# Performance work log

Hardware: AMD Instinct MI355X
Metric: run time of the kernel (lower is better)

The kernel has to match this reference:

```python
import jax, jax.numpy as jnp
import numpy as np

CHUNK = 32  # chunk_size in _delta_rule_chunkwise


def _dwconv_causal(x, filt):
    """Depthwise causal conv. x: [B, L, C], filt: [C, K] -> [B, L, C].
    Matches torch F.conv1d(pad_left=K-1, groups=C) (cross-correlation)."""
    K = filt.shape[-1]
    xc = jnp.transpose(x, (0, 2, 1))  # [B, C, L]
    y = jax.lax.conv_general_dilated(
        xc, filt[:, None, :], (1,), [(K - 1, 0)],
        dimension_numbers=("NCH", "OIH", "NCH"),
        feature_group_count=filt.shape[0])
    return jnp.transpose(y, (0, 2, 1))


def _delta_rule_chunkwise(q, k, v, beta):
    """q,k: [B,H,L,Dk], v: [B,H,L,Dv], beta: [B,H,L]. L % CHUNK == 0."""
    b, h, L, dk = q.shape
    dv = v.shape[-1]
    c = CHUNK
    n = L // c
    q = q * jax.lax.rsqrt(jnp.sum(q * q, -1, keepdims=True))  # l2norm
    k = k * jax.lax.rsqrt(jnp.sum(k * k, -1, keepdims=True))
    v = v * beta[..., None]
    kb = k * beta[..., None]
    qc = q.reshape(b, h, n, c, dk)
    kc = k.reshape(b, h, n, c, dk)
    vc = v.reshape(b, h, n, c, dv)
    kbc = kb.reshape(b, h, n, c, dk)
    # UT transform: T = -(k_beta k^T) strictly-lower, forward substitution, + I
    lower = jnp.tril(jnp.ones((c, c), bool), -1)
    T = -jnp.einsum("bhncd,bhned->bhnce", kbc, kc) * lower
    for i in range(1, c):  # fixed small chunk, sequential dependency
        T = T.at[..., i, :].add(jnp.einsum("bhnj,bhnjk->bhnk", T[..., i, :], T))
    T = T + jnp.eye(c, dtype=T.dtype)
    u = T @ vc   # [b,h,n,c,dv]
    w = T @ kbc  # [b,h,n,c,dk]
    causal = jnp.tril(jnp.ones((c, c), bool))  # incl. diagonal

    def step(S, inp):
        q_i, k_i, u_i, w_i = inp
        attn = jnp.einsum("bhcd,bhed->bhce", q_i, k_i) * causal
        u_t = u_i - w_i @ S
        o_i = q_i @ S + attn @ u_t
        S = S + jnp.einsum("bhcd,bhce->bhde", k_i, u_t)
        return S, o_i

    S0 = jnp.zeros((b, h, dk, dv), q.dtype)
    xs = tuple(jnp.moveaxis(t, 2, 0) for t in (qc, kc, u, w))
    S, o = jax.lax.scan(step, S0, xs)
    o = jnp.moveaxis(o, 0, 2).reshape(b, h, L, dv)
    return o, S


def _rmsnorm(x, weight, eps=1e-5):
    return x * jax.lax.rsqrt(jnp.mean(x * x, -1, keepdims=True) + eps) * weight


def setup_inputs() -> dict:
    B, L, H, NH = 2, 4096, 1024, 4
    DV = H // NH  # 256
    key = jax.random.key(0)
    ks = jax.random.split(key, 14)

    def nrm(k, shape, s=0.02):
        return jax.random.normal(k, shape, jnp.float32) * s

    bf2 = jnp.zeros((NH * 4,), jnp.float32).at[3::4].set(2.0)  # gate_bias_init
    return {
        "hidden_states": jax.random.normal(ks[0], (B, L, H), jnp.float32),
        "Wq": nrm(ks[1], (H, H)), "Wk": nrm(ks[2], (H, H)), "Wv": nrm(ks[3], (H, H)),
        "Wb": nrm(ks[4], (H, NH)),
        "conv_q_w": nrm(ks[5], (H, 4), 0.2),
        "conv_k_w": nrm(ks[6], (H, 4), 0.2),
        "conv_v_w": nrm(ks[7], (H, 4), 0.2),
        "fir_short_w": nrm(ks[8], (NH, DV, 7)),
        "fir_long_w": nrm(ks[9], (NH, DV, 64)),
        "Wf1": nrm(ks[10], (H, 2 * H)), "bf1": jnp.zeros((2 * H,), jnp.float32),
        "Wf2": nrm(ks[11], (2 * H, NH * 4)), "bf2": bf2,
        "rms_w": jnp.ones((DV,), jnp.float32),
        "Wo": nrm(ks[12], (H, H)),
    }


def reference(hidden_states, Wq, Wk, Wv, Wb, conv_q_w, conv_k_w, conv_v_w,
              fir_short_w, fir_long_w, Wf1, bf1, Wf2, bf2, rms_w, Wo):
    B, L, H = hidden_states.shape
    NH, DV, _ = fir_short_w.shape
    DK = H // NH
    # projections + short depthwise causal conv + silu (qk_activation='silu')
    q = jax.nn.silu(_dwconv_causal(hidden_states @ Wq, conv_q_w))
    k = jax.nn.silu(_dwconv_causal(hidden_states @ Wk, conv_k_w))
    v = jax.nn.silu(_dwconv_causal(hidden_states @ Wv, conv_v_w))
    beta = jax.nn.sigmoid(hidden_states @ Wb)  # [B,L,NH]

    q_d = q.reshape(B, L, NH, DK).transpose(0, 2, 1, 3)
    k_d = k.reshape(B, L, NH, DK).transpose(0, 2, 1, 3)
    v4 = v.reshape(B, L, NH, DV)
    v_d = v4.transpose(0, 2, 1, 3)
    beta_d = beta.transpose(0, 2, 1)

    delta_out, _S = _delta_rule_chunkwise(q_d, k_d, v_d, beta_d)
    delta_out = delta_out.transpose(0, 2, 1, 3)  # [B,L,NH,DV]

    # multi-scale depthwise FIR paths on v
    local_short = _dwconv_causal(v4.reshape(B, L, NH * DV),
                                 fir_short_w.reshape(NH * DV, -1)).reshape(B, L, NH, DV)
    local_long = _dwconv_causal(v4.reshape(B, L, NH * DV),
                                fir_long_w.reshape(NH * DV, -1)).reshape(B, L, NH, DV)

    # quad fusion gate: Linear -> GELU -> Linear -> softmax over 4 branches
    h1 = jax.nn.gelu(hidden_states @ Wf1 + bf1, approximate=False)
    fw = jax.nn.softmax((h1 @ Wf2 + bf2).reshape(B, L, NH, 4), axis=-1)

    o = (fw[..., 0:1] * local_short + fw[..., 1:2] * local_long
         + fw[..., 2:3] * delta_out + fw[..., 3:4] * v4)
    o = _rmsnorm(o, rms_w)
    return o.reshape(B, L, NH * DV) @ Wo
```

## Files before the change

### kernel.cpp

```cpp
#include <hip/hip_runtime.h>
#include <cstdint>

typedef __bf16 bf16;
typedef __bf16 bf16x8 __attribute__((ext_vector_type(8)));
typedef __bf16 bf16x4 __attribute__((ext_vector_type(4)));
typedef short  s16x8  __attribute__((ext_vector_type(8)));
typedef float  f32x4  __attribute__((ext_vector_type(4)));

#define DEV __device__ __forceinline__

static const int LL = 4096, HH = 1024, NCH = 128;

DEV float b2f(bf16 x){ return (float)x; }
DEV bf16  f2b(float x){ return (bf16)x; }
DEV f32x4 mfma16(s16x8 a, s16x8 b, f32x4 c){
  return __builtin_amdgcn_mfma_f32_16x16x32_bf16(a, b, c, 0, 0, 0);
}
DEV s16x8 ldg8(const bf16* p){ return *(const s16x8*)p; }

#define LDS_FENCE() do { asm volatile("s_waitcnt lgkmcnt(0)" ::: "memory"); \
                         __builtin_amdgcn_sched_barrier(0); } while(0)

__global__ __launch_bounds__(256) void k_wT(const float* __restrict__ W, bf16* __restrict__ Th,
                                            bf16* __restrict__ Tl, int K, int N){
  __shared__ float Ts[32][33];
  int t = threadIdx.x;
  int ni = blockIdx.x*32, ki = blockIdx.y*32;
  int r = t>>3, c4 = (t&7)*4;
  float4 v = *(const float4*)(W + (size_t)(ki+r)*N + ni + c4);
  Ts[r][c4+0]=v.x; Ts[r][c4+1]=v.y; Ts[r][c4+2]=v.z; Ts[r][c4+3]=v.w;
  __syncthreads();
  bf16x4 hh, llo;
  #pragma unroll
  for(int i=0;i<4;i++){
    float x = Ts[c4+i][r];
    bf16 hb = f2b(x); hh[i]=hb; llo[i]=f2b(x-(float)hb);
  }
  *(bf16x4*)(Th + (size_t)(ni+r)*K + ki + c4) = hh;
  *(bf16x4*)(Tl + (size_t)(ni+r)*K + ki + c4) = llo;
}

template<int EPI, int AF32, int OF32>
__global__ __launch_bounds__(256) void k_gemm_m(const void* __restrict__ Ap,
    const bf16* __restrict__ BTh, const bf16* __restrict__ BTl,
    const float* __restrict__ bias, void* __restrict__ Cp, int M, int N, int K){
  __shared__ __align__(16) bf16 As [128*32];
  __shared__ __align__(16) bf16 Bsh[128*32];
  __shared__ __align__(16) bf16 Bsl[128*32];
  int t = threadIdx.x;
  int w = t>>6, ln = t&63, lr = ln&15, lk = ln>>4;
  int wr = w>>1, wc = w&1;
  int m0 = blockIdx.y*128, n0 = blockIdx.x*128;
  f32x4 acc[4][4];
  #pragma unroll
  for(int m=0;m<4;m++)
    #pragma unroll
    for(int n=0;n<4;n++) acc[m][n] = f32x4{0.f,0.f,0.f,0.f};
  int srow = t>>1, se0 = (t&1)*16;
  int sb0 = srow*64 + ((se0*2     ) ^ ((srow&3)<<4));
  int sb1 = srow*64 + ((se0*2 + 16) ^ ((srow&3)<<4));
  for(int k0=0;k0<K;k0+=32){
    if(AF32){
      const float* Af = (const float*)Ap + (size_t)(m0+srow)*K + k0 + se0;
      float4 p0 = ((const float4*)Af)[0], p1 = ((const float4*)Af)[1];
      float4 p2 = ((const float4*)Af)[2], p3 = ((const float4*)Af)[3];
      bf16x8 v0, v1;
      v0[0]=f2b(p0.x); v0[1]=f2b(p0.y); v0[2]=f2b(p0.z); v0[3]=f2b(p0.w);
      v0[4]=f2b(p1.x); v0[5]=f2b(p1.y); v0[6]=f2b(p1.z); v0[7]=f2b(p1.w);
      v1[0]=f2b(p2.x); v1[1]=f2b(p2.y); v1[2]=f2b(p2.z); v1[3]=f2b(p2.w);
      v1[4]=f2b(p3.x); v1[5]=f2b(p3.y); v1[6]=f2b(p3.z); v1[7]=f2b(p3.w);
      *(bf16x8*)((char*)As + sb0) = v0;
      *(bf16x8*)((char*)As + sb1) = v1;
    } else {
      const bf16* Ab = (const bf16*)Ap + (size_t)(m0+srow)*K + k0 + se0;
      *(bf16x8*)((char*)As + sb0) = *(const bf16x8*)Ab;
      *(bf16x8*)((char*)As + sb1) = *(const bf16x8*)(Ab+8);
    }
    {
      const bf16* bh = BTh + (size_t)(n0+srow)*K + k0 + se0;
      const bf16* bl = BTl + (size_t)(n0+srow)*K + k0 + se0;
      *(bf16x8*)((char*)Bsh + sb0) = *(const bf16x8*)bh;
      *(bf16x8*)((char*)Bsh + sb1) = *(const bf16x8*)(bh+8);
      *(bf16x8*)((char*)Bsl + sb0) = *(const bf16x8*)bl;
      *(bf16x8*)((char*)Bsl + sb1) = *(const bf16x8*)(bl+8);
    }
    __syncthreads();
    s16x8 a[4], bh[4], bl[4];
    #pragma unroll
    for(int m=0;m<4;m++){
      int row = wr*64 + m*16 + lr;
      a[m] = *(const s16x8*)((char*)As + row*64 + ((lk*16) ^ ((lr&3)<<4)));
    }
    #pragma unroll
    for(int n=0;n<4;n++){
      int row = wc*64 + n*16 + lr;
      int off = row*64 + ((lk*16) ^ ((lr&3)<<4));
      bh[n] = *(const s16x8*)((char*)Bsh + off);
      bl[n] = *(const s16x8*)((char*)Bsl + off);
    }
    #pragma unroll
    for(int m=0;m<4;m++)
      #pragma unroll
      for(int n=0;n<4;n++){
        acc[m][n] = mfma16(a[m], bh[n], acc[m][n]);
        acc[m][n] = mfma16(a[m], bl[n], acc[m][n]);
      }
    __syncthreads();
  }
  #pragma unroll
  for(int m=0;m<4;m++)
    #pragma unroll
    for(int n=0;n<4;n++)
      #pragma unroll
      for(int r=0;r<4;r++){
        int gm = m0 + wr*64 + m*16 + lk*4 + r;
        int gn = n0 + wc*64 + n*16 + lr;
        float v = acc[m][n][r];
        if(EPI==1){ v += bias[gn]; v = 0.5f*v*(1.f + erff(v*0.70710678118f)); }
        if(OF32) ((float*)Cp)[(size_t)gm*N + gn] = v;
        else     ((bf16*)Cp)[(size_t)gm*N + gn] = f2b(v);
      }
}

__global__ __launch_bounds__(256) void k_beta(const float* __restrict__ X, const float* __restrict__ Wb,
                                              float* __restrict__ beta){
  int row = blockIdx.x*4 + (threadIdx.x>>6), lane = threadIdx.x&63;
  const float* xp = X + (size_t)row*HH;
  float a0=0,a1=0,a2=0,a3=0;
  for(int k=lane;k<HH;k+=64){
    float x = xp[k];
    float4 wr = *(const float4*)(Wb + (size_t)k*4);
    a0 += x*wr.x; a1 += x*wr.y; a2 += x*wr.z; a3 += x*wr.w;
  }
  #pragma unroll
  for(int off=32;off>=1;off>>=1){
    a0 += __shfl_down(a0,off,64); a1 += __shfl_down(a1,off,64);
    a2 += __shfl_down(a2,off,64); a3 += __shfl_down(a3,off,64);
  }
  if(lane==0){
    beta[(size_t)row*4+0] = 1.f/(1.f+__expf(-a0));
    beta[(size_t)row*4+1] = 1.f/(1.f+__expf(-a1));
    beta[(size_t)row*4+2] = 1.f/(1.f+__expf(-a2));
    beta[(size_t)row*4+3] = 1.f/(1.f+__expf(-a3));
  }
}

__global__ __launch_bounds__(256) void k_conv4(const bf16* __restrict__ pre, const float* __restrict__ filt,
                                               bf16* __restrict__ outp, int do_norm){
  __shared__ float red[4][8];
  int tx = threadIdx.x, head = blockIdx.y, b = blockIdx.z; int l0 = blockIdx.x*64;
  int wv = tx>>6, lane = tx&63;
  int c = head*256 + tx;
  const bf16* p = pre + (size_t)b*LL*HH + c;
  const float* fp = filt + (size_t)c*4;
  float f0=fp[0], f1=fp[1], f2=fp[2], f3=fp[3];
  float x0,x1,x2;
  if(l0>0){ x0=b2f(p[(size_t)(l0-3)*HH]); x1=b2f(p[(size_t)(l0-2)*HH]); x2=b2f(p[(size_t)(l0-1)*HH]); }
  else { x0=x1=x2=0.f; }
  for(int g=0; g<8; g++){
    float y[8];
    #pragma unroll
    for(int i=0;i<8;i++){
      int l = l0+g*8+i;
      float x3 = b2f(p[(size_t)l*HH]);
      float u = f0*x0 + f1*x1 + f2*x2 + f3*x3;
      x0=x1; x1=x2; x2=x3;
      y[i] = u/(1.f+__expf(-u));
    }
    if(do_norm){
      float sq[8];
      #pragma unroll
      for(int i=0;i<8;i++) sq[i]=y[i]*y[i];
      #pragma unroll
      for(int off=32;off>=1;off>>=1)
        #pragma unroll
        for(int i=0;i<8;i++) sq[i] += __shfl_down(sq[i],off,64);
      if(lane==0){
        #pragma unroll
        for(int i=0;i<8;i++) red[wv][i]=sq[i];
      }
      __syncthreads();
      float tot[8];
      #pragma unroll
      for(int i=0;i<8;i++) tot[i]=red[0][i]+red[1][i]+red[2][i]+red[3][i];
      __syncthreads();
      #pragma unroll
      for(int i=0;i<8;i++) y[i] *= rsqrtf(tot[i]);
    }
    #pragma unroll
    for(int i=0;i<8;i++) outp[(size_t)(b*LL + l0+g*8+i)*HH + c] = f2b(y[i]);
  }
}

__global__ __launch_bounds__(256) void k_gate(const bf16* __restrict__ h1, const float* __restrict__ W2,
                                              const float* __restrict__ bf2v, float* __restrict__ fw){
  int row = blockIdx.x*4 + (threadIdx.x>>6), lane = threadIdx.x&63;
  const bf16* hp = h1 + (size_t)row*2048;
  float acc[16];
  #pragma unroll
  for(int c=0;c<16;c++) acc[c]=0.f;
  for(int k=lane;k<2048;k+=64){
    float x = b2f(hp[k]);
    const float* wr = W2 + (size_t)k*16;
    float4 w0 = *(const float4*)(wr), w1 = *(const float4*)(wr+4);
    float4 w2 = *(const float4*)(wr+8), w3 = *(const float4*)(wr+12);
    acc[0]+=x*w0.x; acc[1]+=x*w0.y; acc[2]+=x*w0.z; acc[3]+=x*w0.w;
    acc[4]+=x*w1.x; acc[5]+=x*w1.y; acc[6]+=x*w1.z; acc[7]+=x*w1.w;
    acc[8]+=x*w2.x; acc[9]+=x*w2.y; acc[10]+=x*w2.z; acc[11]+=x*w2.w;
    acc[12]+=x*w3.x; acc[13]+=x*w3.y; acc[14]+=x*w3.z; acc[15]+=x*w3.w;
  }
  #pragma unroll
  for(int off=32;off>=1;off>>=1)
    #pragma unroll
    for(int c=0;c<16;c++) acc[c] += __shfl_down(acc[c],off,64);
  if(lane==0){
    #pragma unroll
    for(int h=0;h<4;h++){
      float s0=acc[h*4+0]+bf2v[h*4+0], s1=acc[h*4+1]+bf2v[h*4+1];
      float s2=acc[h*4+2]+bf2v[h*4+2], s3=acc[h*4+3]+bf2v[h*4+3];
      float mx = fmaxf(fmaxf(s0,s1),fmaxf(s2,s3));
      float e0=__expf(s0-mx), e1=__expf(s1-mx), e2=__expf(s2-mx), e3=__expf(s3-mx);
      float inv = 1.f/(e0+e1+e2+e3);
      fw[(size_t)row*16+h*4+0]=e0*inv; fw[(size_t)row*16+h*4+1]=e1*inv;
      fw[(size_t)row*16+h*4+2]=e2*inv; fw[(size_t)row*16+h*4+3]=e3*inv;
    }
  }
}

__global__ __launch_bounds__(256) void k_pre2(const bf16* __restrict__ qn, const bf16* __restrict__ kn,
    const bf16* __restrict__ vv, const float* __restrict__ beta,
    bf16* __restrict__ uFb, bf16* __restrict__ wFb, bf16* __restrict__ aFb, bf16* __restrict__ aFl,
    bf16* __restrict__ kTb){
  __shared__ __align__(16) bf16 qs[8192], ks[8192], vs[8192];
  __shared__ float T[32][33];
  __shared__ float bet[32];
  int ch = blockIdx.x, bh = blockIdx.y, b = bh>>2, h = bh&3;
  int t = threadIdx.x;
  int l0 = ch*32;
  size_t rowbase = ((size_t)(b*LL+l0))*HH + h*256;
  #pragma unroll
  for(int i=0;i<4;i++){
    int f = i*256+t, row = f>>5, sub = f&31;
    size_t go = rowbase + (size_t)row*HH + sub*8;
    *(bf16x8*)&qs[f*8] = *(const bf16x8*)(qn+go);
    *(bf16x8*)&ks[f*8] = *(const bf16x8*)(kn+go);
    *(bf16x8*)&vs[f*8] = *(const bf16x8*)(vv+go);
  }
  if(t<32) bet[t] = beta[(size_t)(b*LL+l0+t)*4 + h];
  __syncthreads();
  int c = t>>3, e0 = (t&7)*4;
  float d0=0,d1=0,d2=0,d3=0, a0=0,a1=0,a2=0,a3=0;
  for(int d=0; d<256; d++){
    float kc = b2f(ks[c*256+d]);
    float qc = b2f(qs[c*256+d]);
    float k0 = b2f(ks[(e0+0)*256+d]);
    float k1 = b2f(ks[(e0+1)*256+d]);
    float k2 = b2f(ks[(e0+2)*256+d]);
    float k3 = b2f(ks[(e0+3)*256+d]);
    d0 += kc*k0; d1 += kc*k1; d2 += kc*k2; d3 += kc*k3;
    a0 += qc*k0; a1 += qc*k1; a2 += qc*k2; a3 += qc*k3;
  }
  float bc = bet[c];
  T[c][e0+0] = (c>e0+0)? -bc*d0 : 0.f;
  T[c][e0+1] = (c>e0+1)? -bc*d1 : 0.f;
  T[c][e0+2] = (c>e0+2)? -bc*d2 : 0.f;
  T[c][e0+3] = (c>e0+3)? -bc*d3 : 0.f;
  size_t ab = ((size_t)(bh*NCH+ch))*1024;
  {
    float av[4] = { (c>=e0+0)? a0 : 0.f, (c>=e0+1)? a1 : 0.f,
                    (c>=e0+2)? a2 : 0.f, (c>=e0+3)? a3 : 0.f };
    #pragma unroll
    for(int i=0;i<4;i++){
      bf16 hb = f2b(av[i]);
      aFb[ab + c*32 + e0+i] = hb;
      aFl[ab + c*32 + e0+i] = f2b(av[i] - (float)hb);
    }
  }
  __syncthreads();
  if(t < 32){
    volatile float (*Tv)[33] = (volatile float (*)[33])T;
    int j = t;
    for(int i=1;i<32;i++){
      float s2 = 0.f;
      for(int m=0;m<i;m++) s2 += Tv[i][m]*Tv[m][j];
      Tv[i][j] += s2;
    }
    Tv[j][j] += 1.f;
  }
  __syncthreads();
  int dv0 = (t&7)*32;
  float uacc[32], wacc[32];
  #pragma unroll
  for(int j=0;j<32;j++){ uacc[j]=0.f; wacc[j]=0.f; }
  for(int c2=0;c2<32;c2++){
    float coef = T[c][c2]*bet[c2];
    #pragma unroll
    for(int j=0;j<32;j++){
      uacc[j] += coef * b2f(vs[c2*256+dv0+j]);
      wacc[j] += coef * b2f(ks[c2*256+dv0+j]);
    }
  }
  size_t ub = ((size_t)(bh*NCH+ch))*8192 + (size_t)c*256 + dv0;
  #pragma unroll
  for(int j=0;j<32;j++){ uFb[ub+j] = f2b(uacc[j]); wFb[ub+j] = f2b(wacc[j]); }
  {
    bf16* kout = kTb + ((size_t)(bh*NCH+ch))*8192 + (size_t)t*32;
    #pragma unroll
    for(int q8=0;q8<4;q8++){
      bf16x8 v8;
      #pragma unroll
      for(int i=0;i<8;i++) v8[i] = ks[(q8*8+i)*256 + t];
      *(bf16x8*)(kout + q8*8) = v8;
    }
  }
}

__global__ __launch_bounds__(64,1) void k_scan4(const bf16* __restrict__ qn,
    const bf16* __restrict__ wFb, const bf16* __restrict__ uFb,
    const bf16* __restrict__ kTb, const bf16* __restrict__ aFb, const bf16* __restrict__ aFl,
    bf16* __restrict__ delta){
  __shared__ __align__(16) char STh[8192], STl[8192];
  __shared__ __align__(16) char UTh[1024], UTl[1024];
  int l = threadIdx.x;
  int bh = blockIdx.x & 7, js = blockIdx.x >> 3;
  int b = bh>>2, h = bh&3;
  int lr = l & 15, lk = l >> 4;
  int jb = js*16;
  float4 z4 = make_float4(0.f,0.f,0.f,0.f);
  #pragma unroll
  for(int i=0;i<8;i++){ ((float4*)STh)[l+i*64] = z4; ((float4*)STl)[l+i*64] = z4; }
  LDS_FENCE();
  f32x4 Sacc[16];
  #pragma unroll
  for(int i=0;i<16;i++) Sacc[i] = f32x4{0.f,0.f,0.f,0.f};
  const int Xst = (lr&7)<<4;
  const int Xut = (lr&3)<<4;
  const bf16* wp  = wFb + (size_t)bh*NCH*8192;
  const bf16* up  = uFb + (size_t)bh*NCH*8192;
  const bf16* kp  = kTb + (size_t)bh*NCH*8192;
  const bf16* aph = aFb + (size_t)bh*NCH*1024;
  const bf16* apl = aFl + (size_t)bh*NCH*1024;
  const bf16* qp  = qn + (size_t)b*LL*HH + h*256;
  s16x8 Wr[16], Qr[16], Kr[16], A0h, A1h, A0l, A1l;
  bf16 Ur[8];
  #pragma unroll
  for(int t8=0;t8<8;t8++){
    Wr[t8]   = ldg8(wp + lr*256      + t8*32 + lk*8);
    Wr[8+t8] = ldg8(wp + (16+lr)*256 + t8*32 + lk*8);
    Qr[t8]   = ldg8(qp + (size_t)lr*HH      + t8*32 + lk*8);
    Qr[8+t8] = ldg8(qp + (size_t)(16+lr)*HH + t8*32 + lk*8);
  }
  #pragma unroll
  for(int dt=0;dt<16;dt++) Kr[dt] = ldg8(kp + (dt*16+lr)*32 + lk*8);
  A0h = ldg8(aph + lr*32 + lk*8); A1h = ldg8(aph + (16+lr)*32 + lk*8);
  A0l = ldg8(apl + lr*32 + lk*8); A1l = ldg8(apl + (16+lr)*32 + lk*8);
  #pragma unroll
  for(int r8=0;r8<8;r8++){
    int rr = (r8>>2)*16 + lk*4 + (r8&3);
    Ur[r8] = up[(size_t)rr*256 + jb + lr];
  }
  for(int ci=0; ci<NCH; ci++){
    size_t nxw = (ci<NCH-1)? 8192 : 0;
    size_t nxa = (ci<NCH-1)? 1024 : 0;
    size_t nxq = (ci<NCH-1)? (size_t)32*HH : 0;
    f32x4 wh0={0.f,0.f,0.f,0.f}, wl0=wh0, wh1=wh0, wl1=wh0;
    f32x4 qh0=wh0, ql0=wh0, qh1=wh0, ql1=wh0;
    #pragma unroll
    for(int t8=0;t8<8;t8++){
      int ro = lr*512 + ((t8*64 + lk*16) ^ Xst);
      s16x8 sh = *(const s16x8*)(STh + ro);
      s16x8 sl = *(const s16x8*)(STl + ro);
      wh0 = mfma16(Wr[t8],   sh, wh0); wl0 = mfma16(Wr[t8],   sl, wl0);
      wh1 = mfma16(Wr[8+t8], sh, wh1); wl1 = mfma16(Wr[8+t8], sl, wl1);
      qh0 = mfma16(Qr[t8],   sh, qh0); ql0 = mfma16(Qr[t8],   sl, ql0);
      qh1 = mfma16(Qr[8+t8], sh, qh1); ql1 = mfma16(Qr[8+t8], sl, ql1);
    }
    f32x4 ws0 = wh0+wl0, ws1 = wh1+wl1;
    f32x4 qs0 = qh0+ql0, qs1 = qh1+ql1;
    #pragma unroll
    for(int t8=0;t8<8;t8++){
      Wr[t8]   = ldg8(wp + nxw + lr*256      + t8*32 + lk*8);
      Wr[8+t8] = ldg8(wp + nxw + (16+lr)*256 + t8*32 + lk*8);
      Qr[t8]   = ldg8(qp + nxq + (size_t)lr*HH      + t8*32 + lk*8);
      Qr[8+t8] = ldg8(qp + nxq + (size_t)(16+lr)*HH + t8*32 + lk*8);
    }
    #pragma unroll
    for(int ct=0;ct<2;ct++){
      f32x4 w = ct? ws1 : ws0;
      bf16x4 hh, llo;
      #pragma unroll
      for(int r=0;r<4;r++){
        float v = b2f(Ur[ct*4+r]) - w[r];
        bf16 hb = f2b(v); hh[r]=hb; llo[r]=f2b(v-(float)hb);
      }
      int utw = lr*64 + ((ct*32 + lk*8) ^ Xut);
      *(bf16x4*)(UTh+utw)=hh; *(bf16x4*)(UTl+utw)=llo;
    }
    #pragma unroll
    for(int r8=0;r8<8;r8++){
      int rr = (r8>>2)*16 + lk*4 + (r8&3);
      Ur[r8] = up[nxw + (size_t)rr*256 + jb + lr];
    }
    LDS_FENCE();
    int utR = lr*64 + ((lk*16) ^ Xut);
    s16x8 th = *(const s16x8*)(UTh + utR);
    s16x8 tl = *(const s16x8*)(UTl + utR);
    qs0 = mfma16(A0h, th, qs0); qs0 = mfma16(A0h, tl, qs0); qs0 = mfma16(A0l, th, qs0);
    qs1 = mfma16(A1h, th, qs1); qs1 = mfma16(A1h, tl, qs1); qs1 = mfma16(A1l, th, qs1);
    bf16* dp = delta + ((size_t)(b*LL + ci*32))*HH + h*256 + jb + lr;
    #pragma unroll
    for(int ct=0;ct<2;ct++){
      f32x4 o = ct? qs1 : qs0;
      #pragma unroll
      for(int r=0;r<4;r++) dp[(size_t)(ct*16 + lk*4 + r)*HH] = f2b(o[r]);
    }
    A0h = ldg8(aph + nxa + lr*32 + lk*8); A1h = ldg8(aph + nxa + (16+lr)*32 + lk*8);
    A0l = ldg8(apl + nxa + lr*32 + lk*8); A1l = ldg8(apl + nxa + (16+lr)*32 + lk*8);
    #pragma unroll
    for(int dt=0;dt<16;dt++){
      Sacc[dt] = mfma16(Kr[dt], th, Sacc[dt]);
      Sacc[dt] = mfma16(Kr[dt], tl, Sacc[dt]);
    }
    #pragma unroll
    for(int dt=0;dt<16;dt++) Kr[dt] = ldg8(kp + nxw + (size_t)(dt*16+lr)*32 + lk*8);
    #pragma unroll
    for(int dt=0;dt<16;dt++){
      bf16x4 hh, llo;
      #pragma unroll
      for(int r=0;r<4;r++){
        float v = Sacc[dt][r];
        bf16 hb=f2b(v); hh[r]=hb; llo[r]=f2b(v-(float)hb);
      }
      int stw = lr*512 + ((dt*32 + lk*8) ^ Xst);
      *(bf16x4*)(STh+stw)=hh; *(bf16x4*)(STl+stw)=llo;
    }
    LDS_FENCE();
    wp += nxw; up += nxw; kp += nxw; aph += nxa; apl += nxa; qp += nxq;
  }
}

__global__ __launch_bounds__(256) void k_fuse(const bf16* __restrict__ vv, const bf16* __restrict__ delta,
    const float* __restrict__ fw, const float* __restrict__ fsw, const float* __restrict__ flw,
    const float* __restrict__ rmsw, bf16* __restrict__ fused){
  __shared__ float red[4][8];
  int tx = threadIdx.x, head = blockIdx.y, b = blockIdx.z; int l0 = blockIdx.x*64;
  int wv = tx>>6, lane = tx&63;
  int c = head*256 + tx;
  const bf16* vp = vv + (size_t)b*LL*HH + c;
  float fs[7], fl[64];
  #pragma unroll
  for(int j=0;j<7;j++) fs[j] = fsw[(size_t)c*7+j];
  #pragma unroll
  for(int j=0;j<64;j++) fl[j] = flw[(size_t)c*64+j];
  float win[64];
  #pragma unroll
  for(int i=0;i<63;i++){ int l=l0-63+i; win[i] = (l>=0)? b2f(vp[(size_t)l*HH]) : 0.f; }
  float rw = rmsw[tx];
  for(int g=0; g<8; g++){
    float oo[8], sq[8];
    #pragma unroll
    for(int i=0;i<8;i++){
      int s = g*8+i; int l = l0+s;
      win[(s+63)&63] = b2f(vp[(size_t)l*HH]);
      float ll2 = 0.f;
      #pragma unroll
      for(int tp=0;tp<64;tp++) ll2 += fl[tp]*win[(s+tp)&63];
      float ls = 0.f;
      #pragma unroll
      for(int tp=0;tp<7;tp++) ls += fs[tp]*win[(s+57+tp)&63];
      float dl = b2f(delta[(size_t)(b*LL+l)*HH + c]);
      float vh = win[(s+63)&63];
      const float* fp = fw + (size_t)(b*LL+l)*16 + head*4;
      float o = fp[0]*ls + fp[1]*ll2 + fp[2]*dl + fp[3]*vh;
      oo[i]=o; sq[i]=o*o;
    }
    #pragma unroll
    for(int off=32;off>=1;off>>=1)
      #pragma unroll
      for(int i=0;i<8;i++) sq[i] += __shfl_down(sq[i],off,64);
    if(lane==0){
      #pragma unroll
      for(int i=0;i<8;i++) red[wv][i]=sq[i];
    }
    __syncthreads();
    float tot[8];
    #pragma unroll
    for(int i=0;i<8;i++) tot[i]=red[0][i]+red[1][i]+red[2][i]+red[3][i];
    __syncthreads();
    #pragma unroll
    for(int i=0;i<8;i++){
      int l = l0+g*8+i;
      fused[(size_t)(b*LL+l)*HH + c] = f2b(oo[i]*rsqrtf(tot[i]*(1.f/256.f)+1e-5f)*rw);
    }
  }
}

extern "C" void kernel_launch(void* const* d_in, const int* in_sizes, int n_in,
                              void* d_out, int out_size, void* d_ws, size_t ws_size,
                              hipStream_t stream){
  const float* hs  =(const float*)d_in[0];
  const float* Wq  =(const float*)d_in[1];
  const float* Wk  =(const float*)d_in[2];
  const float* Wv  =(const float*)d_in[3];
  const float* Wb  =(const float*)d_in[4];
  const float* cqw =(const float*)d_in[5];
  const float* ckw =(const float*)d_in[6];
  const float* cvw =(const float*)d_in[7];
  const float* fsw =(const float*)d_in[8];
  const float* flw =(const float*)d_in[9];
  const float* Wf1 =(const float*)d_in[10];
  const float* bf1 =(const float*)d_in[11];
  const float* Wf2 =(const float*)d_in[12];
  const float* bf2v=(const float*)d_in[13];
  const float* rmsw=(const float*)d_in[14];
  const float* Wo  =(const float*)d_in[15];

  char* ws = (char*)d_ws;
  size_t off = 0;
  auto alloc = [&](size_t bytes)->char*{
    char* p = ws + off; off = (off + bytes + 255) & ~(size_t)255; return p;
  };
  bf16* pre   = (bf16*)alloc(8192ull*1024*2);
  bf16* qn    = (bf16*)alloc(8192ull*1024*2);
  bf16* kn    = (bf16*)alloc(8192ull*1024*2);
  bf16* vvb   = (bf16*)alloc(8192ull*1024*2);
  float* beta = (float*)alloc(8192ull*4*4);
  bf16* uFb   = (bf16*)alloc(8ull*128*8192*2);
  bf16* wFb   = (bf16*)alloc(8ull*128*8192*2);
  bf16* aFb   = (bf16*)alloc(8ull*128*1024*4);
  float* fw   = (float*)alloc(8192ull*16*4);
  bf16* aFl   = aFb + 8ull*128*1024;
  bf16* h1    = uFb;
  bf16* kTb   = pre;
  bf16* dlt   = (bf16*)d_out;
  bf16* fusedb= pre;
  float* outb = (float*)d_out;
  bf16* WT1h = qn;            bf16* WT1l = qn + 2048ull*1024;
  bf16* WTh  = uFb;           bf16* WTl  = uFb + 1024ull*1024;

  dim3 b256(256);
  k_wT<<<dim3(64,32), b256, 0, stream>>>(Wf1, WT1h, WT1l, 1024, 2048);
  k_gemm_m<1,1,0><<<dim3(16,64), b256, 0, stream>>>(hs, WT1h, WT1l, bf1, h1, 8192, 2048, 1024);
  k_gate<<<dim3(2048), b256, 0, stream>>>(h1, Wf2, bf2v, fw);
  k_wT<<<dim3(32,32), b256, 0, stream>>>(Wq, WTh, WTl, 1024, 1024);
  k_gemm_m<0,1,0><<<dim3(8,64), b256, 0, stream>>>(hs, WTh, WTl, nullptr, pre, 8192, 1024, 1024);
  k_conv4<<<dim3(64,4,2), b256, 0, stream>>>(pre, cqw, qn, 1);
  k_wT<<<dim3(32,32), b256, 0, stream>>>(Wk, WTh, WTl, 1024, 1024);
  k_gemm_m<0,1,0><<<dim3(8,64), b256, 0, stream>>>(hs, WTh, WTl, nullptr, pre, 8192, 1024, 1024);
  k_conv4<<<dim3(64,4,2), b256, 0, stream>>>(pre, ckw, kn, 1);
  k_wT<<<dim3(32,32), b256, 0, stream>>>(Wv, WTh, WTl, 1024, 1024);
  k_gemm_m<0,1,0><<<dim3(8,64), b256, 0, stream>>>(hs, WTh, WTl, nullptr, pre, 8192, 1024, 1024);
  k_conv4<<<dim3(64,4,2), b256, 0, stream>>>(pre, cvw, vvb, 0);
  k_beta<<<dim3(2048), b256, 0, stream>>>(hs, Wb, beta);
  k_pre2<<<dim3(128,8), b256, 0, stream>>>(qn, kn, vvb, beta, uFb, wFb, aFb, aFl, kTb);
  k_scan4<<<dim3(128), dim3(64), 0, stream>>>(qn, wFb, uFb, kTb, aFb, aFl, dlt);
  k_fuse<<<dim3(64,4,2), b256, 0, stream>>>(vvb, dlt, fw, fsw, flw, rmsw, fusedb);
  k_wT<<<dim3(32,32), b256, 0, stream>>>(Wo, WTh, WTl, 1024, 1024);
  k_gemm_m<0,0,1><<<dim3(8,64), b256, 0, stream>>>(fusedb, WTh, WTl, nullptr, outb, 8192, 1024, 1024);

  (void)in_sizes; (void)n_in; (void)out_size; (void)ws_size;
}
```

Before: 1.291 ms.

## Double-buffer GEMM tiles with direct global-to-LDS loads and pre-convert hidden states

Hidden states are converted once to bf16 in a new kernel instead of being converted inside each of four GEMMs. The GEMM now double-buffers its LDS tiles and fills them with global_load_lds (direct global-to-LDS) copies of the next K-slice while MFMAs run on the current one. The scan kernel hoists its LDS reads of the state into registers before the MFMA loop. The costs are extra LDS, one more launch and reliance on the swizzle and barrier ordering staying correct, with only one __syncthreads per iteration.

```diff
diff --git a/kernel.cpp b/kernel.cpp
--- a/kernel.cpp
+++ b/kernel.cpp
@@ -18,8 +18,25 @@
 }
 DEV s16x8 ldg8(const bf16* p){ return *(const s16x8*)p; }
 
+DEV void gld16(const bf16* g, bf16* l){
+  auto* lp = reinterpret_cast<__attribute__((address_space(3))) uint32_t*>(
+      reinterpret_cast<uintptr_t>(l));
+  auto* gp = reinterpret_cast<const __attribute__((address_space(1))) uint32_t*>(
+      reinterpret_cast<uintptr_t>(g));
+  __builtin_amdgcn_global_load_lds(gp, lp, 16, 0, 0);
+}
+
 #define LDS_FENCE() do { asm volatile("s_waitcnt lgkmcnt(0)" ::: "memory"); \
                          __builtin_amdgcn_sched_barrier(0); } while(0)
+
+__global__ __launch_bounds__(256) void k_h2b(const float* __restrict__ X, bf16* __restrict__ Y){
+  size_t i = ((size_t)blockIdx.x*256 + threadIdx.x)*8;
+  float4 a = *(const float4*)(X+i), b = *(const float4*)(X+i+4);
+  bf16x8 v;
+  v[0]=f2b(a.x); v[1]=f2b(a.y); v[2]=f2b(a.z); v[3]=f2b(a.w);
+  v[4]=f2b(b.x); v[5]=f2b(b.y); v[6]=f2b(b.z); v[7]=f2b(b.w);
+  *(bf16x8*)(Y+i) = v;
+}
 
 __global__ __launch_bounds__(256) void k_wT(const float* __restrict__ W, bf16* __restrict__ Th,
                                             bf16* __restrict__ Tl, int K, int N){
@@ -40,13 +57,13 @@
   *(bf16x4*)(Tl + (size_t)(ni+r)*K + ki + c4) = llo;
 }
 
-template<int EPI, int AF32, int OF32>
-__global__ __launch_bounds__(256) void k_gemm_m(const void* __restrict__ Ap,
+template<int EPI, int OF32>
+__global__ __launch_bounds__(256) void k_gemm_m2(const bf16* __restrict__ A,
     const bf16* __restrict__ BTh, const bf16* __restrict__ BTl,
     const float* __restrict__ bias, void* __restrict__ Cp, int M, int N, int K){
-  __shared__ __align__(16) bf16 As [128*32];
-  __shared__ __align__(16) bf16 Bsh[128*32];
-  __shared__ __align__(16) bf16 Bsl[128*32];
+  __shared__ __align__(16) bf16 As [2][128*32];
+  __shared__ __align__(16) bf16 Bsh[2][128*32];
+  __shared__ __align__(16) bf16 Bsl[2][128*32];
   int t = threadIdx.x;
   int w = t>>6, ln = t&63, lr = ln&15, lk = ln>>4;
   int wr = w>>1, wc = w&1;
@@ -56,47 +73,40 @@
   for(int m=0;m<4;m++)
     #pragma unroll
     for(int n=0;n<4;n++) acc[m][n] = f32x4{0.f,0.f,0.f,0.f};
-  int srow = t>>1, se0 = (t&1)*16;
-  int sb0 = srow*64 + ((se0*2     ) ^ ((srow&3)<<4));
-  int sb1 = srow*64 + ((se0*2 + 16) ^ ((srow&3)<<4));
+  int srow[2], gcb[2];
+  #pragma unroll
+  for(int j=0;j<2;j++){
+    srow[j] = w*32 + j*16 + (ln>>2);
+    gcb[j]  = (ln&3) ^ (srow[j]&3);
+  }
+  auto STAGE = [&](int buf, int k0){
+    #pragma unroll
+    for(int j=0;j<2;j++){
+      bf16* lb = &As[buf][(w*32+j*16)*32];
+      gld16(A   + (size_t)(m0+srow[j])*K + k0 + gcb[j]*8, lb);
+      lb = &Bsh[buf][(w*32+j*16)*32];
+      gld16(BTh + (size_t)(n0+srow[j])*K + k0 + gcb[j]*8, lb);
+      lb = &Bsl[buf][(w*32+j*16)*32];
+      gld16(BTl + (size_t)(n0+srow[j])*K + k0 + gcb[j]*8, lb);
+    }
+  };
+  STAGE(0, 0);
+  __syncthreads();
+  int cur = 0;
   for(int k0=0;k0<K;k0+=32){
-    if(AF32){
-      const float* Af = (const float*)Ap + (size_t)(m0+srow)*K + k0 + se0;
-      float4 p0 = ((const float4*)Af)[0], p1 = ((const float4*)Af)[1];
-      float4 p2 = ((const float4*)Af)[2], p3 = ((const float4*)Af)[3];
-      bf16x8 v0, v1;
-      v0[0]=f2b(p0.x); v0[1]=f2b(p0.y); v0[2]=f2b(p0.z); v0[3]=f2b(p0.w);
-      v0[4]=f2b(p1.x); v0[5]=f2b(p1.y); v0[6]=f2b(p1.z); v0[7]=f2b(p1.w);
-      v1[0]=f2b(p2.x); v1[1]=f2b(p2.y); v1[2]=f2b(p2.z); v1[3]=f2b(p2.w);
-      v1[4]=f2b(p3.x); v1[5]=f2b(p3.y); v1[6]=f2b(p3.z); v1[7]=f2b(p3.w);
-      *(bf16x8*)((char*)As + sb0) = v0;
-      *(bf16x8*)((char*)As + sb1) = v1;
-    } else {
-      const bf16* Ab = (const bf16*)Ap + (size_t)(m0+srow)*K + k0 + se0;
-      *(bf16x8*)((char*)As + sb0) = *(const bf16x8*)Ab;
-      *(bf16x8*)((char*)As + sb1) = *(const bf16x8*)(Ab+8);
-    }
-    {
-      const bf16* bh = BTh + (size_t)(n0+srow)*K + k0 + se0;
-      const bf16* bl = BTl + (size_t)(n0+srow)*K + k0 + se0;
-      *(bf16x8*)((char*)Bsh + sb0) = *(const bf16x8*)bh;
-      *(bf16x8*)((char*)Bsh + sb1) = *(const bf16x8*)(bh+8);
-      *(bf16x8*)((char*)Bsl + sb0) = *(const bf16x8*)bl;
-      *(bf16x8*)((char*)Bsl + sb1) = *(const bf16x8*)(bl+8);
-    }
-    __syncthreads();
+    if(k0+32<K) STAGE(cur^1, k0+32);
     s16x8 a[4], bh[4], bl[4];
     #pragma unroll
     for(int m=0;m<4;m++){
       int row = wr*64 + m*16 + lr;
-      a[m] = *(const s16x8*)((char*)As + row*64 + ((lk*16) ^ ((lr&3)<<4)));
+      a[m] = *(const s16x8*)((char*)As[cur] + row*64 + ((lk*16) ^ ((lr&3)<<4)));
     }
     #pragma unroll
     for(int n=0;n<4;n++){
       int row = wc*64 + n*16 + lr;
       int off = row*64 + ((lk*16) ^ ((lr&3)<<4));
-      bh[n] = *(const s16x8*)((char*)Bsh + off);
-      bl[n] = *(const s16x8*)((char*)Bsl + off);
+      bh[n] = *(const s16x8*)((char*)Bsh[cur] + off);
+      bl[n] = *(const s16x8*)((char*)Bsl[cur] + off);
     }
     #pragma unroll
     for(int m=0;m<4;m++)
@@ -106,6 +116,7 @@
         acc[m][n] = mfma16(a[m], bl[n], acc[m][n]);
       }
     __syncthreads();
+    cur ^= 1;
   }
   #pragma unroll
   for(int m=0;m<4;m++)
@@ -363,17 +374,21 @@
     size_t nxw = (ci<NCH-1)? 8192 : 0;
     size_t nxa = (ci<NCH-1)? 1024 : 0;
     size_t nxq = (ci<NCH-1)? (size_t)32*HH : 0;
+    s16x8 sth[8], stl[8];
+    #pragma unroll
+    for(int t8=0;t8<8;t8++){
+      int ro = lr*512 + ((t8*64 + lk*16) ^ Xst);
+      sth[t8] = *(const s16x8*)(STh + ro);
+      stl[t8] = *(const s16x8*)(STl + ro);
+    }
     f32x4 wh0={0.f,0.f,0.f,0.f}, wl0=wh0, wh1=wh0, wl1=wh0;
     f32x4 qh0=wh0, ql0=wh0, qh1=wh0, ql1=wh0;
     #pragma unroll
     for(int t8=0;t8<8;t8++){
-      int ro = lr*512 + ((t8*64 + lk*16) ^ Xst);
-      s16x8 sh = *(const s16x8*)(STh + ro);
-      s16x8 sl = *(const s16x8*)(STl + ro);
-      wh0 = mfma16(Wr[t8],   sh, wh0); wl0 = mfma16(Wr[t8],   sl, wl0);
-      wh1 = mfma16(Wr[8+t8], sh, wh1); wl1 = mfma16(Wr[8+t8], sl, wl1);
-      qh0 = mfma16(Qr[t8],   sh, qh0); ql0 = mfma16(Qr[t8],   sl, ql0);
-      qh1 = mfma16(Qr[8+t8], sh, qh1); ql1 = mfma16(Qr[8+t8], sl, ql1);
+      wh0 = mfma16(Wr[t8],   sth[t8], wh0); wl0 = mfma16(Wr[t8],   stl[t8], wl0);
+      wh1 = mfma16(Wr[8+t8], sth[t8], wh1); wl1 = mfma16(Wr[8+t8], stl[t8], wl1);
+      qh0 = mfma16(Qr[t8],   sth[t8], qh0); ql0 = mfma16(Qr[t8],   stl[t8], ql0);
+      qh1 = mfma16(Qr[8+t8], sth[t8], qh1); ql1 = mfma16(Qr[8+t8], stl[t8], ql1);
     }
     f32x4 ws0 = wh0+wl0, ws1 = wh1+wl1;
     f32x4 qs0 = qh0+ql0, qs1 = qh1+ql1;
@@ -535,28 +550,30 @@
   bf16* dlt   = (bf16*)d_out;
   bf16* fusedb= pre;
   float* outb = (float*)d_out;
+  bf16* hsb  = vvb;
   bf16* WT1h = qn;            bf16* WT1l = qn + 2048ull*1024;
   bf16* WTh  = uFb;           bf16* WTl  = uFb + 1024ull*1024;
 
   dim3 b256(256);
+  k_h2b<<<dim3(4096), b256, 0, stream>>>(hs, hsb);
   k_wT<<<dim3(64,32), b256, 0, stream>>>(Wf1, WT1h, WT1l, 1024, 2048);
-  k_gemm_m<1,1,0><<<dim3(16,64), b256, 0, stream>>>(hs, WT1h, WT1l, bf1, h1, 8192, 2048, 1024);
+  k_gemm_m2<1,0><<<dim3(16,64), b256, 0, stream>>>(hsb, WT1h, WT1l, bf1, h1, 8192, 2048, 1024);
   k_gate<<<dim3(2048), b256, 0, stream>>>(h1, Wf2, bf2v, fw);
   k_wT<<<dim3(32,32), b256, 0, stream>>>(Wq, WTh, WTl, 1024, 1024);
-  k_gemm_m<0,1,0><<<dim3(8,64), b256, 0, stream>>>(hs, WTh, WTl, nullptr, pre, 8192, 1024, 1024);
+  k_gemm_m2<0,0><<<dim3(8,64), b256, 0, stream>>>(hsb, WTh, WTl, nullptr, pre, 8192, 1024, 1024);
   k_conv4<<<dim3(64,4,2), b256, 0, stream>>>(pre, cqw, qn, 1);
   k_wT<<<dim3(32,32), b256, 0, stream>>>(Wk, WTh, WTl, 1024, 1024);
-  k_gemm_m<0,1,0><<<dim3(8,64), b256, 0, stream>>>(hs, WTh, WTl, nullptr, pre, 8192, 1024, 1024);
+  k_gemm_m2<0,0><<<dim3(8,64), b256, 0, stream>>>(hsb, WTh, WTl, nullptr, pre, 8192, 1024, 1024);
   k_conv4<<<dim3(64,4,2), b256, 0, stream>>>(pre, ckw, kn, 1);
   k_wT<<<dim3(32,32), b256, 0, stream>>>(Wv, WTh, WTl, 1024, 1024);
-  k_gemm_m<0,1,0><<<dim3(8,64), b256, 0, stream>>>(hs, WTh, WTl, nullptr, pre, 8192, 1024, 1024);
+  k_gemm_m2<0,0><<<dim3(8,64), b256, 0, stream>>>(hsb, WTh, WTl, nullptr, pre, 8192, 1024, 1024);
   k_conv4<<<dim3(64,4,2), b256, 0, stream>>>(pre, cvw, vvb, 0);
   k_beta<<<dim3(2048), b256, 0, stream>>>(hs, Wb, beta);
   k_pre2<<<dim3(128,8), b256, 0, stream>>>(qn, kn, vvb, beta, uFb, wFb, aFb, aFl, kTb);
   k_scan4<<<dim3(128), dim3(64), 0, stream>>>(qn, wFb, uFb, kTb, aFb, aFl, dlt);
   k_fuse<<<dim3(64,4,2), b256, 0, stream>>>(vvb, dlt, fw, fsw, flw, rmsw, fusedb);
   k_wT<<<dim3(32,32), b256, 0, stream>>>(Wo, WTh, WTl, 1024, 1024);
-  k_gemm_m<0,0,1><<<dim3(8,64), b256, 0, stream>>>(fusedb, WTh, WTl, nullptr, outb, 8192, 1024, 1024);
+  k_gemm_m2<0,1><<<dim3(8,64), b256, 0, stream>>>(fusedb, WTh, WTl, nullptr, outb, 8192, 1024, 1024);
 
   (void)in_sizes; (void)n_in; (void)out_size; (void)ws_size;
 }
```

New measurement: 1.199 ms. -7.1%, faster.
